# Kernel optimization log

Hardware: AMD Instinct MI355X
Metric: run time of the kernel (lower is better)

The kernel has to match this reference:

```python
import jax, jax.numpy as jnp
import numpy as np

C_A = 768; C_S = 384; C_Z = 128; H = 16; D = C_A // H
B = 1; N = 4096; NQ = 32; NK = 128; NB = N // NQ
EPS = 1e-5


def _ln(x):
    # layernorm without learned affine (affine applied by caller where present)
    m = jnp.mean(x, axis=-1, keepdims=True)
    v = jnp.mean((x - m) ** 2, axis=-1, keepdims=True)
    return (x - m) * jax.lax.rsqrt(v + EPS)


def setup_inputs() -> dict:
    key = jax.random.key(0)
    ks = jax.random.split(key, 16)
    w = lambda k, shp: jax.random.normal(k, shp, dtype=jnp.float32) * 0.02
    return dict(
        a=jax.random.normal(ks[0], (B, N, C_A), jnp.float32),
        s=jax.random.normal(ks[1], (B, N, C_S), jnp.float32),
        z=jax.random.normal(ks[2], (B, NB, NQ, NK, C_Z), jnp.float32),
        adaln_gamma_s=jnp.ones((C_S,), jnp.float32),
        adaln_ws=w(ks[3], (C_S, C_A)),
        adaln_bs=jnp.zeros((C_A,), jnp.float32),
        adaln_wskip=w(ks[4], (C_S, C_A)),
        lnz_gamma=jnp.ones((C_Z,), jnp.float32),
        wz=w(ks[5], (C_Z, H)),
        wq=w(ks[6], (C_A, C_A)), bq=jnp.zeros((C_A,), jnp.float32),
        wk=w(ks[7], (C_A, C_A)),
        wv=w(ks[8], (C_A, C_A)),
        wg=w(ks[9], (C_A, C_A)), bg=jnp.ones((C_A,), jnp.float32),
        wo=w(ks[10], (C_A, C_A)), bo=jnp.zeros((C_A,), jnp.float32),
        w_last=w(ks[11], (C_S, C_A)),
        b_last=jnp.full((C_A,), -2.0, jnp.float32),  # biasinit = -2.0
        n_queries=NQ, n_keys=NK,
    )


def _forward(a, s, z, adaln_gamma_s, adaln_ws, adaln_bs, adaln_wskip,
             lnz_gamma, wz, wq, bq, wk, wv, wg, bg, wo, bo,
             w_last, b_last, n_queries, n_keys):
    Bq, Nq, _ = a.shape
    nb = Nq // n_queries
    # AdaptiveLayerNorm (AF3 Alg 26): a <- sigmoid(Lin(s_ln)) * LN(a) + LinNoBias(s_ln)
    s_ln = _ln(s) * adaln_gamma_s
    a_ln = jax.nn.sigmoid(s_ln @ adaln_ws + adaln_bs) * _ln(a) + s_ln @ adaln_wskip
    # pair bias: LN(z) (no offset) -> per-head bias, permuted to [B,H,nb,nq,nk]
    bias = (_ln(z) * lnz_gamma) @ wz                    # [B, nb, nq, nk, H]
    bias = jnp.transpose(bias, (0, 4, 1, 2, 3))          # [B, H, nb, nq, nk]
    # projections (q has bias; k/v no bias)
    q = (a_ln @ wq + bq).reshape(Bq, nb, n_queries, H, D)
    k = (a_ln @ wk).reshape(Bq, Nq, H, D)
    v = (a_ln @ wv).reshape(Bq, Nq, H, D)
    # local window: query block w covers [w*nq, (w+1)*nq); keys are nk centered on it
    start = jnp.arange(nb) * n_queries + n_queries // 2 - n_keys // 2
    kidx = start[:, None] + jnp.arange(n_keys)[None, :]  # [nb, nk]
    valid = (kidx >= 0) & (kidx < Nq)
    kidx = jnp.clip(kidx, 0, Nq - 1)
    k_loc = k[:, kidx]                                    # [B, nb, nk, H, D]
    v_loc = v[:, kidx]
    scale = 1.0 / float(np.sqrt(D))
    scores = jnp.einsum('bwqhd,bwkhd->bhwqk', q, k_loc) * scale + bias
    scores = jnp.where(valid[None, None, :, None, :], scores, -1e9)
    p = jax.nn.softmax(scores, axis=-1)
    o = jnp.einsum('bhwqk,bwkhd->bwqhd', p, v_loc).reshape(Bq, Nq, C_A)
    # gating, output projection, final sigmoid gate from raw s
    o = (jax.nn.sigmoid(a_ln @ wg + bg) * o) @ wo + bo
    return jax.nn.sigmoid(s @ w_last + b_last) * o


def reference(a, s, z, adaln_gamma_s, adaln_ws, adaln_bs, adaln_wskip,
              lnz_gamma, wz, wq, bq, wk, wv, wg, bg, wo, bo,
              w_last, b_last, n_queries, n_keys):
    return _forward(a, s, z, adaln_gamma_s, adaln_ws, adaln_bs, adaln_wskip,
                    lnz_gamma, wz, wq, bq, wk, wv, wg, bg, wo, bo,
                    w_last, b_last, n_queries, n_keys)
```

## Files before the change

### kernel.cpp

```cpp
#include <hip/hip_runtime.h>
#include <hip/hip_bf16.h>
#include <math.h>

#define N_TOK 4096
#define CA 768
#define CS 384
#define CZ 128
#define NHEAD 16
#define DH 48
#define NQW 32
#define NKW 128
#define NBLK 128

typedef __attribute__((ext_vector_type(8))) short short8;
typedef __attribute__((ext_vector_type(4))) float float4v;
typedef __attribute__((ext_vector_type(4))) unsigned short ushort4v;

__device__ __forceinline__ float sigmoidf_(float x){ return 1.0f/(1.0f+__expf(-x)); }

__device__ __forceinline__ unsigned short f2bf(float x){
  unsigned u = __float_as_uint(x);
  unsigned r = (u + 0x7FFFu + ((u>>16)&1u)) >> 16;
  return (unsigned short)r;
}
__device__ __forceinline__ float bf2f(unsigned short b){
  return __uint_as_float(((unsigned)b)<<16);
}
__device__ __forceinline__ short8 cvt8(const float* xv){
  union { short8 v; unsigned short u[8]; } H;
  #pragma unroll
  for (int j=0;j<8;j++) H.u[j] = f2bf(xv[j]);
  return H.v;
}
__device__ __forceinline__ short8 cvt8pk(const float* x){
  union { short8 v; unsigned u32[4]; } H;
  #pragma unroll
  for (int i=0;i<4;i++)
    asm("v_cvt_pk_bf16_f32 %0, %1, %2" : "=v"(H.u32[i]) : "v"(x[2*i]), "v"(x[2*i+1]));
  return H.v;
}

__device__ __forceinline__ void gload_lds16(const void* gsrc, void* ldst){
  __builtin_amdgcn_global_load_lds(
    (const __attribute__((address_space(1))) void*)gsrc,
    (__attribute__((address_space(3))) void*)ldst, 16, 0, 0);
}

__device__ __forceinline__ int xcd_swz(int wg, int nwg){
  int cpx = nwg >> 3;
  return (wg & 7)*cpx + (wg >> 3);
}

__global__ __launch_bounds__(256) void prep_zbias_kernel(
  const float* __restrict__ z, const float* __restrict__ lnz_gamma,
  const float* __restrict__ wz, unsigned short* __restrict__ bias3,
  const float* __restrict__ s, const float* __restrict__ adaln_gamma,
  unsigned short* __restrict__ s_ln_h, unsigned short* __restrict__ s_h,
  const float* __restrict__ a, float* __restrict__ a_n,
  const float* __restrict__ ws, const float* __restrict__ wskip,
  const float* __restrict__ wq, const float* __restrict__ wk,
  const float* __restrict__ wv, const float* __restrict__ wg,
  const float* __restrict__ wo, const float* __restrict__ wlast,
  unsigned short* __restrict__ Wt1, unsigned short* __restrict__ Wt2,
  unsigned short* __restrict__ Wt3, unsigned short* __restrict__ Wt4,
  const float* __restrict__ bq, const float* __restrict__ bg,
  float* __restrict__ biasq)
{
  union PZ {
    float tile[64][65];
    float zbuf[2][2][2048];
  };
  __shared__ PZ sm;
  int bid = blockIdx.x;
  int tid = threadIdx.x;

  if (bid < 2048){
    int wave = tid>>6, lane = tid&63;
    if (wave >= 2) return;
    int lr = lane&15, quad = lane>>4;

    short8 bwh[4];
    float w1 = 0.f;
    #pragma unroll
    for (int ks=0;ks<4;ks++){
      float wv_[8];
      #pragma unroll
      for (int j=0;j<8;j++){
        int k = ks*32 + quad*8 + j;
        wv_[j] = wz[k*NHEAD + lr]*lnz_gamma[k];
        w1 += wv_[j];
      }
      bwh[ks] = cvt8pk(wv_);
    }
    w1 += __shfl_xor(w1, 16);
    w1 += __shfl_xor(w1, 32);

    size_t group = (size_t)bid*2 + wave;
    const float* zg = z + group*(size_t)(NKW*CZ);
    unsigned short* outg = bias3 + group*2048;

    int rsub = lane>>5;
    int csw  = lane&31;
    auto stage = [&](int buf, int b){
      #pragma unroll
      for (int i=0;i<8;i++){
        int r  = 2*i + rsub;
        int gc = csw ^ (r & 7);
        gload_lds16(zg + (size_t)(b*16 + r)*CZ + gc*4, &sm.zbuf[wave][buf][i*256]);
      }
    };

    stage(0, 0);
    int buf = 0;
    #pragma unroll 1
    for (int b=0; b<8; ++b){
      if (b < 7){
        stage(buf^1, b+1);
        asm volatile("s_waitcnt vmcnt(8)" ::: "memory");
      } else {
        asm volatile("s_waitcnt vmcnt(0)" ::: "memory");
      }
      __builtin_amdgcn_sched_barrier(0);

      const float* rowp = &sm.zbuf[wave][buf][lr*128];
      int sswz = lr & 7;
      float4 p[8];
      #pragma unroll
      for (int ks=0;ks<4;ks++){
        int c0 = ks*8 + quad*2;
        p[ks*2]   = *(const float4*)(rowp + (size_t)((c0  )^sswz)*4);
        p[ks*2+1] = *(const float4*)(rowp + (size_t)((c0+1)^sswz)*4);
      }
      float sum=0.f, sq=0.f;
      #pragma unroll
      for (int t=0;t<8;t++){
        sum += p[t].x + p[t].y + p[t].z + p[t].w;
        sq  += p[t].x*p[t].x + p[t].y*p[t].y + p[t].z*p[t].z + p[t].w*p[t].w;
      }
      sum += __shfl_xor(sum,16); sum += __shfl_xor(sum,32);
      sq  += __shfl_xor(sq,16);  sq  += __shfl_xor(sq,32);
      float mean = sum*(1.f/CZ);
      float var  = sq*(1.f/CZ) - mean*mean;
      float rs = rsqrtf(var + 1e-5f);

      float4v c = (float4v){0.f,0.f,0.f,0.f};
      #pragma unroll
      for (int ks=0;ks<4;ks++){
        float xv[8];
        xv[0]=p[ks*2].x;   xv[1]=p[ks*2].y;   xv[2]=p[ks*2].z;   xv[3]=p[ks*2].w;
        xv[4]=p[ks*2+1].x; xv[5]=p[ks*2+1].y; xv[6]=p[ks*2+1].z; xv[7]=p[ks*2+1].w;
        c = __builtin_amdgcn_mfma_f32_16x16x32_bf16(cvt8pk(xv), bwh[ks], c, 0,0,0);
      }

      ushort4v o4;
      #pragma unroll
      for (int r=0;r<4;r++){
        int rrow = quad*4 + r;
        float m_r  = __shfl(mean, rrow);
        float rs_r = __shfl(rs, rrow);
        o4[r] = f2bf(rs_r*(c[r] - m_r*w1));
      }
      *(ushort4v*)(outg + lr*128 + b*16 + quad*4) = o4;
      buf ^= 1;
    }
    return;
  }
  bid -= 2048;

  if (bid < 1024){
    int wave = tid>>6, lane = tid&63;
    int row = bid*4 + wave;
    const float* x = s + (size_t)row*CS;
    float v[6]; float sum=0.f, sq=0.f;
    #pragma unroll
    for (int i=0;i<6;i++){ v[i]=x[lane+64*i]; sum+=v[i]; sq+=v[i]*v[i]; }
    #pragma unroll
    for (int off=32; off; off>>=1){ sum+=__shfl_xor(sum,off); sq+=__shfl_xor(sq,off); }
    float m = sum*(1.f/CS);
    float var = sq*(1.f/CS)-m*m;
    float rs = rsqrtf(var+1e-5f);
    #pragma unroll
    for (int i=0;i<6;i++){
      int c = lane+64*i;
      s_ln_h[(size_t)row*CS+c] = f2bf((v[i]-m)*rs*adaln_gamma[c]);
      s_h[(size_t)row*CS+c]    = f2bf(v[i]);
    }
    return;
  }
  bid -= 1024;

  if (bid < 1024){
    int wave = tid>>6, lane = tid&63;
    int row = bid*4 + wave;
    const float* x = a + (size_t)row*CA;
    float v[12]; float sum=0.f, sq=0.f;
    #pragma unroll
    for (int i=0;i<12;i++){ v[i]=x[lane+64*i]; sum+=v[i]; sq+=v[i]*v[i]; }
    #pragma unroll
    for (int off=32; off; off>>=1){ sum+=__shfl_xor(sum,off); sq+=__shfl_xor(sq,off); }
    float m = sum*(1.f/CA);
    float var = sq*(1.f/CA)-m*m;
    float rs = rsqrtf(var+1e-5f);
    float* o = a_n + (size_t)row*CA;
    #pragma unroll
    for (int i=0;i<12;i++) o[lane+64*i] = (v[i]-m)*rs;
    return;
  }
  bid -= 1024;

  if (bid < 936){
    const float* src; unsigned short* dst; int K; int local;
    if      (bid < 72)  { src=ws;    dst=Wt1;                   K=CS; local=bid; }
    else if (bid < 144) { src=wskip; dst=Wt1 + (size_t)768*CS;  K=CS; local=bid-72; }
    else if (bid < 288) { src=wq;    dst=Wt2;                   K=CA; local=bid-144; }
    else if (bid < 432) { src=wk;    dst=Wt2 + (size_t)768*CA;  K=CA; local=bid-288; }
    else if (bid < 576) { src=wv;    dst=Wt2 + (size_t)1536*CA; K=CA; local=bid-432; }
    else if (bid < 720) { src=wg;    dst=Wt2 + (size_t)2304*CA; K=CA; local=bid-576; }
    else if (bid < 864) { src=wo;    dst=Wt3;                   K=CA; local=bid-720; }
    else                { src=wlast; dst=Wt4;                   K=CS; local=bid-864; }
    int ktiles = K/64;
    int kb = (local % ktiles)*64, nb = (local / ktiles)*64;
    int c = tid & 63, r0 = tid >> 6;
    #pragma unroll
    for (int i=0;i<16;i++){
      int r = r0 + 4*i;
      sm.tile[r][c] = src[(size_t)(kb+r)*CA + nb + c];
    }
    __syncthreads();
    #pragma unroll
    for (int i=0;i<16;i++){
      int r = r0 + 4*i;
      dst[(size_t)(nb+r)*K + kb + c] = f2bf(sm.tile[c][r]);
    }
    return;
  }
  bid -= 936;

  int i = bid*256 + tid;
  float v = 0.f;
  if (i < 768) v = bq[i];
  else if (i >= 2304) v = bg[i-2304];
  biasq[i] = v;
}

__global__ __launch_bounds__(256) void adaln_gemm(
  const unsigned short* __restrict__ A, const unsigned short* __restrict__ Bt,
  const float* __restrict__ bs, const float* __restrict__ a_n,
  unsigned short* __restrict__ outh)
{
  __shared__ unsigned short Ash[64*64];
  __shared__ unsigned short B1sh[128*64];
  __shared__ unsigned short B2sh[128*64];

  int tid = threadIdx.x;
  int w = tid >> 6, lane = tid & 63;
  int lr = lane & 15, quad = lane >> 4;
  int wg = xcd_swz(blockIdx.y*gridDim.x + blockIdx.x, gridDim.x*gridDim.y);
  int bx = wg % gridDim.x, by = wg / gridDim.x;
  int m0 = by*64, n0 = bx*128;
  int mbase = (w&1)*32, nbase = (w>>1)*64;

  float4v acc1[2][4], acc2[2][4];
  #pragma unroll
  for (int i=0;i<2;i++)
    #pragma unroll
    for (int j=0;j<4;j++){
      acc1[i][j] = (float4v){0.f,0.f,0.f,0.f};
      acc2[i][j] = (float4v){0.f,0.f,0.f,0.f};
    }

  int rsub = lane>>3;
  int gcs  = ((lane&7) ^ rsub)*8;
  int rkey = lr & 7;

  for (int k0=0; k0<CS; k0+=64){
    __syncthreads();
    #pragma unroll
    for (int it=0; it<2; ++it){
      int r = it*32 + w*8 + rsub;
      gload_lds16(A + (size_t)(m0 + r)*CS + k0 + gcs, &Ash[(it*32 + w*8)*64]);
    }
    #pragma unroll
    for (int it=0; it<4; ++it){
      int r = it*32 + w*8 + rsub;
      gload_lds16(Bt + (size_t)(n0 + r)*CS + k0 + gcs, &B1sh[(it*32 + w*8)*64]);
      gload_lds16(Bt + (size_t)(768 + n0 + r)*CS + k0 + gcs, &B2sh[(it*32 + w*8)*64]);
    }
    __syncthreads();

    #pragma unroll
    for (int ks=0; ks<2; ++ks){
      int slot = ((ks*4 + quad) ^ rkey)*8;
      short8 af[2], b1f[4], b2f[4];
      #pragma unroll
      for (int mi=0;mi<2;mi++)
        af[mi] = *(const short8*)&Ash[(mbase + mi*16 + lr)*64 + slot];
      #pragma unroll
      for (int ni=0;ni<4;ni++){
        b1f[ni] = *(const short8*)&B1sh[(nbase + ni*16 + lr)*64 + slot];
        b2f[ni] = *(const short8*)&B2sh[(nbase + ni*16 + lr)*64 + slot];
      }
      #pragma unroll
      for (int mi=0;mi<2;mi++)
        #pragma unroll
        for (int ni=0;ni<4;ni++){
          acc1[mi][ni] = __builtin_amdgcn_mfma_f32_16x16x32_bf16(af[mi], b1f[ni], acc1[mi][ni], 0,0,0);
          acc2[mi][ni] = __builtin_amdgcn_mfma_f32_16x16x32_bf16(af[mi], b2f[ni], acc2[mi][ni], 0,0,0);
        }
    }
  }

  #pragma unroll
  for (int ni=0;ni<4;ni++){
    int col = n0 + nbase + ni*16 + lr;
    float bsv = bs[col];
    #pragma unroll
    for (int mi=0;mi<2;mi++){
      #pragma unroll
      for (int reg=0;reg<4;reg++){
        int row = m0 + mbase + mi*16 + quad*4 + reg;
        float v = sigmoidf_(acc1[mi][ni][reg] + bsv)*a_n[(size_t)row*CA + col] + acc2[mi][ni][reg];
        outh[(size_t)row*CA + col] = f2bf(v);
      }
    }
  }
}

__global__ __launch_bounds__(256) void final_gemm(
  const unsigned short* __restrict__ A1, const unsigned short* __restrict__ B1,
  const float* __restrict__ bias1,
  const unsigned short* __restrict__ A2, const unsigned short* __restrict__ B2,
  const float* __restrict__ bias2,
  float* __restrict__ outp)
{
  __shared__ unsigned short Ash[64*64];
  __shared__ unsigned short Bsh[128*64];

  int tid = threadIdx.x;
  int w = tid >> 6, lane = tid & 63;
  int lr = lane & 15, quad = lane >> 4;
  int wg = xcd_swz(blockIdx.y*gridDim.x + blockIdx.x, gridDim.x*gridDim.y);
  int bx = wg % gridDim.x, by = wg / gridDim.x;
  int m0 = by*64, n0 = bx*128;
  int mbase = (w&1)*32, nbase = (w>>1)*64;

  float4v acc1[2][4], acc2[2][4];
  #pragma unroll
  for (int i=0;i<2;i++)
    #pragma unroll
    for (int j=0;j<4;j++){
      acc1[i][j] = (float4v){0.f,0.f,0.f,0.f};
      acc2[i][j] = (float4v){0.f,0.f,0.f,0.f};
    }

  int rsub = lane>>3;
  int gcs  = ((lane&7) ^ rsub)*8;
  int rkey = lr & 7;

  const int NT1 = CA/64, NT2 = CS/64, NT = NT1+NT2;
  #pragma unroll 1
  for (int t=0; t<NT; ++t){
    const unsigned short* Ap; const unsigned short* Bp; int K, k0;
    if (t < NT1){ Ap=A1; Bp=B1; K=CA; k0=t*64; }
    else        { Ap=A2; Bp=B2; K=CS; k0=(t-NT1)*64; }
    __syncthreads();
    #pragma unroll
    for (int it=0; it<2; ++it){
      int r = it*32 + w*8 + rsub;
      gload_lds16(Ap + (size_t)(m0 + r)*K + k0 + gcs, &Ash[(it*32 + w*8)*64]);
    }
    #pragma unroll
    for (int it=0; it<4; ++it){
      int r = it*32 + w*8 + rsub;
      gload_lds16(Bp + (size_t)(n0 + r)*K + k0 + gcs, &Bsh[(it*32 + w*8)*64]);
    }
    __syncthreads();

    #pragma unroll
    for (int ks=0; ks<2; ++ks){
      int slot = ((ks*4 + quad) ^ rkey)*8;
      short8 af[2], bf[4];
      #pragma unroll
      for (int mi=0;mi<2;mi++)
        af[mi] = *(const short8*)&Ash[(mbase + mi*16 + lr)*64 + slot];
      #pragma unroll
      for (int ni=0;ni<4;ni++)
        bf[ni] = *(const short8*)&Bsh[(nbase + ni*16 + lr)*64 + slot];
      if (t < NT1){
        #pragma unroll
        for (int mi=0;mi<2;mi++)
          #pragma unroll
          for (int ni=0;ni<4;ni++)
            acc1[mi][ni] = __builtin_amdgcn_mfma_f32_16x16x32_bf16(af[mi], bf[ni], acc1[mi][ni], 0,0,0);
      } else {
        #pragma unroll
        for (int mi=0;mi<2;mi++)
          #pragma unroll
          for (int ni=0;ni<4;ni++)
            acc2[mi][ni] = __builtin_amdgcn_mfma_f32_16x16x32_bf16(af[mi], bf[ni], acc2[mi][ni], 0,0,0);
      }
    }
  }

  #pragma unroll
  for (int ni=0;ni<4;ni++){
    int col = n0 + nbase + ni*16 + lr;
    float bv1 = bias1[col];
    float bv2 = bias2[col];
    #pragma unroll
    for (int mi=0;mi<2;mi++){
      #pragma unroll
      for (int reg=0;reg<4;reg++){
        int row = m0 + mbase + mi*16 + quad*4 + reg;
        outp[(size_t)row*CA + col] = sigmoidf_(acc2[mi][ni][reg] + bv2)*(acc1[mi][ni][reg] + bv1);
      }
    }
  }
}

__global__ __launch_bounds__(256) void qkvg_gemm(
  const unsigned short* __restrict__ A1, const unsigned short* __restrict__ B1,
  const float* __restrict__ bias1, unsigned short* __restrict__ outp)
{
  __shared__ unsigned short Ash[128*64];
  __shared__ unsigned short Bsh[128*64];

  int tid = threadIdx.x;
  int w = tid >> 6, lane = tid & 63;
  int lr = lane & 15, quad = lane >> 4;
  int wg = xcd_swz(blockIdx.y*gridDim.x + blockIdx.x, gridDim.x*gridDim.y);
  int bx = wg % gridDim.x, by = wg / gridDim.x;
  int m0 = by*128, n0 = bx*128;
  int mbase = (w&1)*64, nbase = (w>>1)*64;

  float4v acc1[4][4];
  #pragma unroll
  for (int i=0;i<4;i++)
    #pragma unroll
    for (int j=0;j<4;j++)
      acc1[i][j] = (float4v){0.f,0.f,0.f,0.f};

  int rsub = lane>>3;
  int gcs  = ((lane&7) ^ rsub)*8;
  int rkey = lr & 7;

  for (int k0=0; k0<CA; k0+=64){
    __syncthreads();
    #pragma unroll
    for (int it=0; it<4; ++it){
      int r = it*32 + w*8 + rsub;
      gload_lds16(A1 + (size_t)(m0 + r)*CA + k0 + gcs, &Ash[(it*32 + w*8)*64]);
      gload_lds16(B1 + (size_t)(n0 + r)*CA + k0 + gcs, &Bsh[(it*32 + w*8)*64]);
    }
    __syncthreads();

    #pragma unroll
    for (int ks=0; ks<2; ++ks){
      int slot = ((ks*4 + quad) ^ rkey)*8;
      short8 af[4], bf[4];
      #pragma unroll
      for (int mi=0;mi<4;mi++)
        af[mi] = *(const short8*)&Ash[(mbase + mi*16 + lr)*64 + slot];
      #pragma unroll
      for (int ni=0;ni<4;ni++)
        bf[ni] = *(const short8*)&Bsh[(nbase + ni*16 + lr)*64 + slot];
      #pragma unroll
      for (int mi=0;mi<4;mi++)
        #pragma unroll
        for (int ni=0;ni<4;ni++)
          acc1[mi][ni] = __builtin_amdgcn_mfma_f32_16x16x32_bf16(af[mi], bf[ni], acc1[mi][ni], 0,0,0);
    }
  }

  #pragma unroll
  for (int ni=0;ni<4;ni++){
    int col = n0 + nbase + ni*16 + lr;
    float bv = bias1[col];
    #pragma unroll
    for (int mi=0;mi<4;mi++){
      #pragma unroll
      for (int reg=0;reg<4;reg++){
        int row = m0 + mbase + mi*16 + quad*4 + reg;
        outp[(size_t)row*3072 + col] = f2bf(acc1[mi][ni][reg] + bv);
      }
    }
  }
}

__global__ __launch_bounds__(256) void attn_kernel(
  const unsigned short* __restrict__ qh,
  const unsigned short* __restrict__ bias3h,
  unsigned short* __restrict__ og)
{
  __shared__ unsigned short Vs[128*192];
  __shared__ unsigned short Pb[4][32*40];
  int tid = threadIdx.x, wave = tid>>6, lane = tid&63;
  int lr = lane&15, quad = lane>>4;
  int w = blockIdx.x, h = blockIdx.y*4 + wave;
  int start = w*NQW - 48;
  const float scale = 0.14433756729740643f;

  {
    int hbase = blockIdx.y*4*DH;
    #pragma unroll
    for (int it=0; it<12; ++it){
      int c = it*256 + tid;
      int key = c/24, cc = c - key*24;
      int kr = min(max(start+key,0),N_TOK-1);
      short8 v = *(const short8*)&qh[(size_t)kr*3072 + 1536 + hbase + cc*8];
      int cs = cc ^ (((key>>3)&3)*2);
      *(short8*)&Vs[key*192 + cs*8] = v;
    }
  }

  short8 zero8 = {0,0,0,0,0,0,0,0};

  short8 aq[2][2];
  #pragma unroll
  for (int mt=0;mt<2;mt++){
    int row = w*NQW + mt*16 + lr;
    const unsigned short* qp = qh + (size_t)row*3072 + h*DH;
    aq[mt][0] = *(const short8*)(qp + quad*8);
    aq[mt][1] = (quad<2) ? *(const short8*)(qp + 32 + quad*8) : zero8;
  }

  float4v c[2][8];
  #pragma unroll
  for (int mt=0;mt<2;mt++)
    #pragma unroll
    for (int nt=0;nt<8;nt++) c[mt][nt] = (float4v){0.f,0.f,0.f,0.f};

  #pragma unroll 2
  for (int nt=0;nt<8;nt++){
    int krc = min(max(start + nt*16 + lr,0),N_TOK-1);
    const unsigned short* kp = qh + (size_t)krc*3072 + 768 + h*DH;
    short8 bk0 = *(const short8*)(kp + quad*8);
    short8 bk1 = (quad<2) ? *(const short8*)(kp + 32 + quad*8) : zero8;
    #pragma unroll
    for (int mt=0;mt<2;mt++){
      c[mt][nt] = __builtin_amdgcn_mfma_f32_16x16x32_bf16(aq[mt][0], bk0, c[mt][nt], 0,0,0);
      c[mt][nt] = __builtin_amdgcn_mfma_f32_16x16x32_bf16(aq[mt][1], bk1, c[mt][nt], 0,0,0);
    }
  }

  float rmax[2][4], rsum[2][4];
  #pragma unroll
  for (int mt=0;mt<2;mt++)
    #pragma unroll
    for (int r=0;r<4;r++){ rmax[mt][r] = -3.0e38f; rsum[mt][r] = 0.f; }

  #pragma unroll
  for (int nt=0;nt<8;nt++){
    int key = start + nt*16 + lr;
    bool valid = (key>=0) && (key<N_TOK);
    #pragma unroll
    for (int mt=0;mt<2;mt++){
      #pragma unroll
      for (int r=0;r<4;r++){
        int q = mt*16 + quad*4 + r;
        float bv = bf2f(bias3h[(((size_t)(w*NQW+q))*NHEAD + h)*128 + nt*16 + lr]);
        float v = valid ? (c[mt][nt][r]*scale + bv) : -1e9f;
        c[mt][nt][r] = v;
        rmax[mt][r] = fmaxf(rmax[mt][r], v);
      }
    }
  }
  #pragma unroll
  for (int mt=0;mt<2;mt++)
    #pragma unroll
    for (int r=0;r<4;r++){
      float m = rmax[mt][r];
      m = fmaxf(m, __shfl_xor(m,1)); m = fmaxf(m, __shfl_xor(m,2));
      m = fmaxf(m, __shfl_xor(m,4)); m = fmaxf(m, __shfl_xor(m,8));
      rmax[mt][r] = m;
    }
  #pragma unroll
  for (int nt=0;nt<8;nt++)
    #pragma unroll
    for (int mt=0;mt<2;mt++)
      #pragma unroll
      for (int r=0;r<4;r++){
        float e = __expf(c[mt][nt][r] - rmax[mt][r]);
        c[mt][nt][r] = e;
        rsum[mt][r] += e;
      }
  #pragma unroll
  for (int mt=0;mt<2;mt++)
    #pragma unroll
    for (int r=0;r<4;r++){
      float sv = rsum[mt][r];
      sv += __shfl_xor(sv,1); sv += __shfl_xor(sv,2);
      sv += __shfl_xor(sv,4); sv += __shfl_xor(sv,8);
      rsum[mt][r] = 1.f/sv;
    }

  __syncthreads();

  unsigned short* ph = &Pb[wave][0];
  float4v o[2][3];
  #pragma unroll
  for (int mt=0;mt<2;mt++)
    #pragma unroll
    for (int no=0;no<3;no++) o[mt][no] = (float4v){0.f,0.f,0.f,0.f};

  #pragma unroll 1
  for (int c2=0;c2<2;c2++){
    #pragma unroll 1
    for (int ks=0;ks<2;ks++){
      int ntb = c2*4 + ks*2;
      #pragma unroll
      for (int t=0;t<2;t++){
        int nt = ntb + t;
        #pragma unroll
        for (int mt=0;mt<2;mt++){
          #pragma unroll
          for (int r=0;r<4;r++){
            int q = mt*16 + quad*4 + r;
            ph[q*40 + t*16 + lr] = f2bf(c[mt][nt][r]*rsum[mt][r]);
          }
        }
      }
      short8 pa[2];
      #pragma unroll
      for (int mt=0;mt<2;mt++)
        pa[mt] = *(const short8*)&ph[(mt*16+lr)*40 + quad*8];
      #pragma unroll
      for (int no=0;no<3;no++){
        union { short8 v; unsigned short u[8]; } V;
        int col = wave*DH + no*16 + lr;
        int chunk = col >> 3;
        int cs = (chunk ^ (quad*2))*8 + (col & 7);
        #pragma unroll
        for (int j=0;j<8;j++){
          int key = c2*64 + ks*32 + quad*8 + j;
          V.u[j] = Vs[key*192 + cs];
        }
        #pragma unroll
        for (int mt=0;mt<2;mt++)
          o[mt][no] = __builtin_amdgcn_mfma_f32_16x16x32_bf16(pa[mt], V.v, o[mt][no], 0,0,0);
      }
    }
  }

  #pragma unroll
  for (int mt=0;mt<2;mt++){
    #pragma unroll
    for (int no=0;no<3;no++){
      int d = no*16 + lr;
      #pragma unroll
      for (int r=0;r<4;r++){
        int q = mt*16 + quad*4 + r;
        size_t grow = (size_t)(w*NQW + q);
        float g = bf2f(qh[grow*3072 + 2304 + h*DH + d]);
        og[grow*CA + h*DH + d] = f2bf(o[mt][no][r] * sigmoidf_(g));
      }
    }
  }
}

extern "C" void kernel_launch(void* const* d_in, const int* in_sizes, int n_in,
                              void* d_out, int out_size, void* d_ws, size_t ws_size,
                              hipStream_t stream)
{
  const float* a            = (const float*)d_in[0];
  const float* s            = (const float*)d_in[1];
  const float* z            = (const float*)d_in[2];
  const float* adaln_gamma  = (const float*)d_in[3];
  const float* adaln_ws     = (const float*)d_in[4];
  const float* adaln_bs     = (const float*)d_in[5];
  const float* adaln_wskip  = (const float*)d_in[6];
  const float* lnz_gamma    = (const float*)d_in[7];
  const float* wz           = (const float*)d_in[8];
  const float* wq           = (const float*)d_in[9];
  const float* bq           = (const float*)d_in[10];
  const float* wk           = (const float*)d_in[11];
  const float* wv           = (const float*)d_in[12];
  const float* wg           = (const float*)d_in[13];
  const float* bg           = (const float*)d_in[14];
  const float* wo           = (const float*)d_in[15];
  const float* bo           = (const float*)d_in[16];
  const float* w_last       = (const float*)d_in[17];
  const float* b_last       = (const float*)d_in[18];
  float* out = (float*)d_out;

  char* base = (char*)d_ws;
  size_t off = 0;
  auto alloc = [&](size_t bytes)->char*{ char* p = base + off; off += (bytes + 255) & ~(size_t)255; return p; };

  unsigned short* s_ln_h = (unsigned short*)alloc((size_t)N_TOK*CS*2);
  unsigned short* s_h    = (unsigned short*)alloc((size_t)N_TOK*CS*2);
  float*          a_n    = (float*)alloc((size_t)N_TOK*CA*4);
  unsigned short* a_ln_h = (unsigned short*)alloc((size_t)N_TOK*CA*2);
  unsigned short* og_h   = (unsigned short*)alloc((size_t)N_TOK*CA*2);
  unsigned short* Wt1    = (unsigned short*)alloc((size_t)1536*CS*2);
  unsigned short* Wt2    = (unsigned short*)alloc((size_t)3072*CA*2);
  unsigned short* Wt3    = (unsigned short*)alloc((size_t)CA*CA*2);
  unsigned short* Wt4    = (unsigned short*)alloc((size_t)CA*CS*2);
  unsigned short* bias3h = (unsigned short*)alloc((size_t)N_TOK*NHEAD*NKW*2);
  unsigned short* qkvg_h = (unsigned short*)alloc((size_t)N_TOK*3072*2);
  float*          biasq  = (float*)alloc((size_t)3072*4);

  prep_zbias_kernel<<<dim3(2048+1024+1024+936+12), 256, 0, stream>>>(
      z, lnz_gamma, wz, bias3h,
      s, adaln_gamma, s_ln_h, s_h, a, a_n,
      adaln_ws, adaln_wskip, wq, wk, wv, wg, wo, w_last,
      Wt1, Wt2, Wt3, Wt4, bq, bg, biasq);

  adaln_gemm<<<dim3(CA/128, N_TOK/64), 256, 0, stream>>>(s_ln_h, Wt1, adaln_bs, a_n, a_ln_h);

  qkvg_gemm<<<dim3(3072/128, N_TOK/128), 256, 0, stream>>>(a_ln_h, Wt2, biasq, qkvg_h);

  attn_kernel<<<dim3(NBLK, 4), 256, 0, stream>>>(qkvg_h, bias3h, og_h);

  final_gemm<<<dim3(CA/128, N_TOK/64), 256, 0, stream>>>(
      og_h, Wt3, bo, s_h, Wt4, b_last, out);
}
```

Measured before the change: 217.5 us.

## Use 256x256 double-buffered tiles with 512 threads in QKVG GEMM

Replaces the 128x128 single-buffered QKVG GEMM with a 256x256 tile, 8 waves of 128x64 each, and a two-stage LDS double buffer. Global-to-LDS loads for step t+2 are issued while step t is computed, with explicit vmcnt waits and barriers. The aim is to hide load latency and raise data reuse per tile. In exchange it uses 128KB of LDS and more accumulators per wave, and the grid drops to 192 blocks, which underfills 256 CUs.

```diff
diff --git a/kernel.cpp b/kernel.cpp
--- a/kernel.cpp
+++ b/kernel.cpp
@@ -418,70 +418,85 @@
   }
 }
 
-__global__ __launch_bounds__(256) void qkvg_gemm(
+__global__ __launch_bounds__(512) void qkvg_gemm256(
   const unsigned short* __restrict__ A1, const unsigned short* __restrict__ B1,
   const float* __restrict__ bias1, unsigned short* __restrict__ outp)
 {
-  __shared__ unsigned short Ash[128*64];
-  __shared__ unsigned short Bsh[128*64];
+  __shared__ unsigned short Ash[2][256*64];
+  __shared__ unsigned short Bsh[2][256*64];
 
   int tid = threadIdx.x;
-  int w = tid >> 6, lane = tid & 63;
+  int v = tid >> 6, lane = tid & 63;
   int lr = lane & 15, quad = lane >> 4;
   int wg = xcd_swz(blockIdx.y*gridDim.x + blockIdx.x, gridDim.x*gridDim.y);
   int bx = wg % gridDim.x, by = wg / gridDim.x;
-  int m0 = by*128, n0 = bx*128;
-  int mbase = (w&1)*64, nbase = (w>>1)*64;
-
-  float4v acc1[4][4];
-  #pragma unroll
-  for (int i=0;i<4;i++)
+  int m0 = by*256, n0 = bx*256;
+  int wr = (v>>2)*128;
+  int wc = (v&3)*64;
+
+  float4v acc[8][4];
+  #pragma unroll
+  for (int i=0;i<8;i++)
     #pragma unroll
     for (int j=0;j<4;j++)
-      acc1[i][j] = (float4v){0.f,0.f,0.f,0.f};
+      acc[i][j] = (float4v){0.f,0.f,0.f,0.f};
 
   int rsub = lane>>3;
   int gcs  = ((lane&7) ^ rsub)*8;
   int rkey = lr & 7;
 
-  for (int k0=0; k0<CA; k0+=64){
-    __syncthreads();
-    #pragma unroll
-    for (int it=0; it<4; ++it){
-      int r = it*32 + w*8 + rsub;
-      gload_lds16(A1 + (size_t)(m0 + r)*CA + k0 + gcs, &Ash[(it*32 + w*8)*64]);
-      gload_lds16(B1 + (size_t)(n0 + r)*CA + k0 + gcs, &Bsh[(it*32 + w*8)*64]);
-    }
-    __syncthreads();
-
+  const int NT = CA/64;
+
+  auto stage = [&](int buf, int t){
+    int k0 = t*64;
+    #pragma unroll
+    for (int i=0;i<4;i++){
+      int R = i*64 + v*8;
+      gload_lds16(A1 + (size_t)(m0 + R + rsub)*CA + k0 + gcs, &Ash[buf][R*64]);
+      gload_lds16(B1 + (size_t)(n0 + R + rsub)*CA + k0 + gcs, &Bsh[buf][R*64]);
+    }
+  };
+
+  stage(0, 0);
+  stage(1, 1);
+  int cur = 0;
+  #pragma unroll 1
+  for (int t=0; t<NT; ++t){
+    if (t+1 < NT) asm volatile("s_waitcnt vmcnt(8)" ::: "memory");
+    else          asm volatile("s_waitcnt vmcnt(0)" ::: "memory");
+    __builtin_amdgcn_sched_barrier(0);
+    __builtin_amdgcn_s_barrier();
     #pragma unroll
     for (int ks=0; ks<2; ++ks){
       int slot = ((ks*4 + quad) ^ rkey)*8;
-      short8 af[4], bf[4];
-      #pragma unroll
-      for (int mi=0;mi<4;mi++)
-        af[mi] = *(const short8*)&Ash[(mbase + mi*16 + lr)*64 + slot];
+      short8 af[8], bf[4];
+      #pragma unroll
+      for (int mi=0;mi<8;mi++)
+        af[mi] = *(const short8*)&Ash[cur][(wr + mi*16 + lr)*64 + slot];
       #pragma unroll
       for (int ni=0;ni<4;ni++)
-        bf[ni] = *(const short8*)&Bsh[(nbase + ni*16 + lr)*64 + slot];
-      #pragma unroll
-      for (int mi=0;mi<4;mi++)
+        bf[ni] = *(const short8*)&Bsh[cur][(wc + ni*16 + lr)*64 + slot];
+      #pragma unroll
+      for (int mi=0;mi<8;mi++)
         #pragma unroll
         for (int ni=0;ni<4;ni++)
-          acc1[mi][ni] = __builtin_amdgcn_mfma_f32_16x16x32_bf16(af[mi], bf[ni], acc1[mi][ni], 0,0,0);
-    }
+          acc[mi][ni] = __builtin_amdgcn_mfma_f32_16x16x32_bf16(af[mi], bf[ni], acc[mi][ni], 0,0,0);
+    }
+    __builtin_amdgcn_s_barrier();
+    if (t+2 < NT) stage(cur, t+2);
+    cur ^= 1;
   }
 
   #pragma unroll
   for (int ni=0;ni<4;ni++){
-    int col = n0 + nbase + ni*16 + lr;
+    int col = n0 + wc + ni*16 + lr;
     float bv = bias1[col];
     #pragma unroll
-    for (int mi=0;mi<4;mi++){
+    for (int mi=0;mi<8;mi++){
       #pragma unroll
       for (int reg=0;reg<4;reg++){
-        int row = m0 + mbase + mi*16 + quad*4 + reg;
-        outp[(size_t)row*3072 + col] = f2bf(acc1[mi][ni][reg] + bv);
+        int row = m0 + wr + mi*16 + quad*4 + reg;
+        outp[(size_t)row*3072 + col] = f2bf(acc[mi][ni][reg] + bv);
       }
     }
   }
@@ -708,7 +723,7 @@
 
   adaln_gemm<<<dim3(CA/128, N_TOK/64), 256, 0, stream>>>(s_ln_h, Wt1, adaln_bs, a_n, a_ln_h);
 
-  qkvg_gemm<<<dim3(3072/128, N_TOK/128), 256, 0, stream>>>(a_ln_h, Wt2, biasq, qkvg_h);
+  qkvg_gemm256<<<dim3(3072/256, N_TOK/256), 512, 0, stream>>>(a_ln_h, Wt2, biasq, qkvg_h);
 
   attn_kernel<<<dim3(NBLK, 4), 256, 0, stream>>>(qkvg_h, bias3h, og_h);
 
```

Result: no change. 217.6 us (median of 2 runs) (+0.0%).
